# Kernel optimization log

Measured on AMD Instinct MI355X. Metric: run time of the kernel, lower is better.

Reference implementation:

```python
import jax, jax.numpy as jnp
import numpy as np
import math

EMBED = 256
NH = 8      # num_heads
NP = 4      # num_points
HD = EMBED // NH  # head_dim = 32
BS = 8
NQ = 8192
HH = 128
WW = 128


def setup_inputs() -> dict:
    key = jax.random.key(0)
    ks = jax.random.split(key, 12)
    query = jax.random.normal(ks[0], (BS, NQ, EMBED), jnp.float32)
    reference_points = jax.random.uniform(ks[1], (BS, NQ, 2), dtype=jnp.float32)
    value = jax.random.normal(ks[2], (BS, HH * WW, EMBED), jnp.float32)
    # sampling_offsets: torch init uses zero weight + structured bias (rose pattern);
    # use small random weight so the math path is exercised, keep the structured bias.
    w_off = 0.001 * jax.random.normal(ks[3], (EMBED, NH * NP * 2), jnp.float32)
    thetas = np.arange(NH, dtype=np.float32) * (2.0 * math.pi / NH)
    grid = np.stack([np.cos(thetas), np.sin(thetas)], -1)          # [NH, 2]
    grid = np.tile(grid[:, None, :], (1, NP, 1)) * np.arange(1, NP + 1, dtype=np.float32)[None, :, None]
    b_off = jnp.asarray(grid.reshape(-1), jnp.float32)              # [NH*NP*2]
    w_attn = 0.01 * jax.random.normal(ks[4], (EMBED, NH * NP), jnp.float32)
    b_attn = jnp.zeros((NH * NP,), jnp.float32)
    xav = 1.0 / math.sqrt(EMBED)
    w_val = xav * jax.random.normal(ks[5], (EMBED, EMBED), jnp.float32)
    b_val = jnp.zeros((EMBED,), jnp.float32)
    w_out = xav * jax.random.normal(ks[6], (EMBED, EMBED), jnp.float32)
    b_out = jnp.zeros((EMBED,), jnp.float32)
    return {"query": query, "reference_points": reference_points, "value": value,
            "w_off": w_off, "b_off": b_off, "w_attn": w_attn, "b_attn": b_attn,
            "w_val": w_val, "b_val": b_val, "w_out": w_out, "b_out": b_out,
            "H": HH, "W": WW}


def _deform_attn(query, reference_points, value, w_off, b_off, w_attn, b_attn,
                 w_val, b_val, w_out, b_out, H, W):
    bs, nq, _ = query.shape
    # value projection -> [bs, nh, H*W, hd]
    v = (value @ w_val + b_val).reshape(bs, H * W, NH, HD).transpose(0, 2, 1, 3)
    # offsets and attention weights
    off = (query @ w_off + b_off).reshape(bs, nq, NH, NP, 2)
    attn = jax.nn.softmax((query @ w_attn + b_attn).reshape(bs, nq, NH, NP), axis=-1)
    norm = jnp.array([W, H], dtype=query.dtype)
    loc = reference_points[:, :, None, None, :] + off / norm       # [bs,nq,nh,np,2] in [0,1]
    # grid_sample, align_corners=False: pixel = loc*size - 0.5  (x <-> W, y <-> H)
    px = (loc[..., 0] * W - 0.5).transpose(0, 2, 1, 3).reshape(bs, NH, nq * NP)
    py = (loc[..., 1] * H - 0.5).transpose(0, 2, 1, 3).reshape(bs, NH, nq * NP)
    x0 = jnp.floor(px); y0 = jnp.floor(py)
    wx = px - x0; wy = py - y0
    x0i = x0.astype(jnp.int32); y0i = y0.astype(jnp.int32)

    def gather(xi, yi):
        # padding_mode='zeros': out-of-range corners contribute 0
        mask = ((xi >= 0) & (xi < W) & (yi >= 0) & (yi < H)).astype(v.dtype)
        idx = jnp.clip(yi, 0, H - 1) * W + jnp.clip(xi, 0, W - 1)   # [bs,nh,K]
        g = jnp.take_along_axis(v, idx[..., None], axis=2)          # [bs,nh,K,hd]
        return g * mask[..., None]

    samp = (((1 - wx) * (1 - wy))[..., None] * gather(x0i, y0i)
            + (wx * (1 - wy))[..., None] * gather(x0i + 1, y0i)
            + ((1 - wx) * wy)[..., None] * gather(x0i, y0i + 1)
            + (wx * wy)[..., None] * gather(x0i + 1, y0i + 1))      # [bs,nh,nq*np,hd]
    samp = samp.reshape(bs, NH, nq, NP, HD)
    aw = attn.transpose(0, 2, 1, 3)                                 # [bs,nh,nq,np]
    out = jnp.einsum('bhqpd,bhqp->bqhd', samp, aw).reshape(bs, nq, EMBED)
    return out @ w_out + b_out


def reference(query, reference_points, value, w_off, b_off, w_attn, b_attn,
              w_val, b_val, w_out, b_out, H, W):
    return _deform_attn(query, reference_points, value, w_off, b_off, w_attn, b_attn,
                        w_val, b_val, w_out, b_out, H, W)
```

## Files before the change

kernel.cpp:

```cpp
#include <hip/hip_runtime.h>
#include <stdint.h>

#define NQ 8192
#define BSZ 8
#define NH 8
#define NP 4
#define HD 32
#define EMBED 256
#define IMG 128
#define NPIX (IMG*IMG)

typedef __attribute__((ext_vector_type(8))) short short8v;
typedef __attribute__((ext_vector_type(4))) float f32x4;

static __device__ __forceinline__ float bf2f(uint32_t u) {
    union { uint32_t i; float f; } x; x.i = u << 16; return x.f;
}
static __device__ __forceinline__ uint16_t f2bf(float f) {
    union { float f; uint32_t i; } x; x.f = f;
    uint32_t r = x.i + 0x7fffu + ((x.i >> 16) & 1u);
    return (uint16_t)(r >> 16);
}
static __device__ __forceinline__ uint32_t cvtpk(float lo, float hi) {
    uint32_t r;
    asm("v_cvt_pk_bf16_f32 %0, %1, %2" : "=v"(r) : "v"(lo), "v"(hi));
    return r;
}
static __device__ __forceinline__ void gload_lds16(const void* g, void* l) {
    __builtin_amdgcn_global_load_lds(
        (const __attribute__((address_space(1))) unsigned int*)g,
        (__attribute__((address_space(3))) unsigned int*)l, 16, 0, 0);
}

#define WAITV(n) asm volatile("s_waitcnt vmcnt(" #n ")" ::: "memory")
#define WAITLGKM() do { asm volatile("s_waitcnt lgkmcnt(0)" ::: "memory"); \
                        __builtin_amdgcn_sched_barrier(0); } while (0)
#define BARRIER() do { __builtin_amdgcn_s_barrier(); \
                       __builtin_amdgcn_sched_barrier(0); } while (0)

static __device__ __forceinline__ void waitv_n(int n) {
    switch (n) {
        case 0: WAITV(0); break;  case 1: WAITV(1); break;
        case 2: WAITV(2); break;  case 3: WAITV(3); break;
        case 4: WAITV(4); break;  case 5: WAITV(5); break;
        case 6: WAITV(6); break;  case 8: WAITV(8); break;
        default: WAITV(10); break;
    }
}

__global__ void pack_w(const float* __restrict__ w_val, const float* __restrict__ w_out,
                       const float* __restrict__ w_off, const float* __restrict__ w_attn,
                       uint16_t* __restrict__ wTval, uint16_t* __restrict__ wTout,
                       uint16_t* __restrict__ wTcat) {
    int k = blockIdx.x;
    int n = threadIdx.x;
    wTval[n * 256 + k] = f2bf(w_val[k * 256 + n]);
    wTout[n * 256 + k] = f2bf(w_out[k * 256 + n]);
    if (n < 64)       wTcat[n * 256 + k]        = f2bf(w_off[k * 64 + n]);
    else if (n < 96)  wTcat[n * 256 + k]        = f2bf(w_attn[k * 32 + (n - 64)]);
}

template<bool A_F32, bool OUT_F32, bool PLANE, int STRIPES>
__global__ __launch_bounds__(512, 2)
void gemm_pk(const void* __restrict__ Ap, const uint16_t* __restrict__ BT,
             void* __restrict__ Cp, const float* __restrict__ bias) {
    constexpr int TILEB = A_F32 ? 16384 : 8192;
    constexpr int NR    = 131072 / TILEB;
    constexpr int T     = STRIPES * 4;
    constexpr int LPT   = A_F32 ? 2 : 1;
    __shared__ char SMEM[131072 + (PLANE ? 32768 : 0)];
    char* ring = SMEM;
    const int tid = threadIdx.x, w = tid >> 6, l = tid & 63;
    const int stripe0 = blockIdx.x * STRIPES;

    auto stageA = [&](int slot, int t) {
        const int gr0 = (stripe0 + (t >> 2)) * 64 + (t & 3) * 16;
        if constexpr (A_F32) {
#pragma unroll
            for (int c = 0; c < 2; ++c) {
                int loff = c * 8192 + tid * 16;
                int row = loff >> 10, x = loff & 1023;
                const char* src = (const char*)Ap + (size_t)(gr0 + row) * 1024
                                  + (x ^ ((row & 7) << 4));
                gload_lds16(src, ring + slot * 16384 + c * 8192 + w * 1024);
            }
        } else {
            int loff = tid * 16;
            int row = loff >> 9, x = loff & 511;
            const char* src = (const char*)Ap + (size_t)(gr0 + row) * 512
                              + (x ^ ((row & 7) << 4));
            gload_lds16(src, ring + slot * 8192 + w * 1024);
        }
    };

#pragma unroll
    for (int c = 0; c < 16; ++c) {
        int loff = c * 8192 + tid * 16;
        int row = loff >> 9, x = loff & 511;
        const char* src = (const char*)BT + (size_t)row * 512 + (x ^ ((row & 7) << 4));
        gload_lds16(src, SMEM + c * 8192 + w * 1024);
    }
    WAITV(0);
    BARRIER();
    short8v breg[2][8];
#pragma unroll
    for (int n = 0; n < 2; ++n) {
        int col = w * 32 + n * 16 + (l & 15);
        const char* base = SMEM + col * 512;
        const int sz = (col & 7) << 4;
#pragma unroll
        for (int k = 0; k < 8; ++k)
            breg[n][k] = *(const short8v*)(base + ((k * 64 + (l >> 4) * 16) ^ sz));
    }
    WAITLGKM();
    BARRIER();
#pragma unroll
    for (int t = 0; t < 6; ++t) stageA(t & (NR - 1), t);

    for (int st = 0; st < STRIPES; ++st) {
        f32x4 acc[4][2] = {};
#pragma unroll
        for (int s = 0; s < 4; ++s) {
            const int t = st * 4 + s;
            const int rem = T - 1 - t;
            waitv_n((rem < 5 ? rem : 5) * LPT);
            BARRIER();
            if (t + 6 < T) stageA((t + 6) & (NR - 1), t + 6);
            const int slot = t & (NR - 1);
            short8v a[8];
            const int sz = (l & 7) << 4;
            if constexpr (A_F32) {
                const char* base = ring + slot * 16384 + (l & 15) * 1024;
#pragma unroll
                for (int k = 0; k < 8; ++k) {
                    int off = k * 128 + (l >> 4) * 32;
                    f32x4 lo = *(const f32x4*)(base + (off ^ sz));
                    f32x4 hi = *(const f32x4*)(base + ((off + 16) ^ sz));
                    union { uint32_t u[4]; short8v s8; } pk;
                    pk.u[0] = cvtpk(lo[0], lo[1]); pk.u[1] = cvtpk(lo[2], lo[3]);
                    pk.u[2] = cvtpk(hi[0], hi[1]); pk.u[3] = cvtpk(hi[2], hi[3]);
                    a[k] = pk.s8;
                }
            } else {
                const char* base = ring + slot * 8192 + (l & 15) * 512;
#pragma unroll
                for (int k = 0; k < 8; ++k)
                    a[k] = *(const short8v*)(base + ((k * 64 + (l >> 4) * 16) ^ sz));
            }
#pragma unroll
            for (int k = 0; k < 8; ++k)
#pragma unroll
                for (int n = 0; n < 2; ++n)
                    acc[s][n] = __builtin_amdgcn_mfma_f32_16x16x32_bf16(a[k], breg[n][k], acc[s][n], 0, 0, 0);
        }

        const int gr0 = (stripe0 + st) * 64;
        if constexpr (PLANE) {
            char* Cs = SMEM + 131072;
#pragma unroll
            for (int s = 0; s < 4; ++s)
#pragma unroll
                for (int n = 0; n < 2; ++n) {
                    int lcol = w * 32 + n * 16 + (l & 15);
                    float bv = bias[lcol];
#pragma unroll
                    for (int r = 0; r < 4; ++r) {
                        int lrow = s * 16 + (l >> 4) * 4 + r;
                        *(uint16_t*)(Cs + ((lrow * 512 + lcol * 2) ^ ((lrow & 7) << 4)))
                            = f2bf(acc[s][n][r] + bv);
                    }
                }
            WAITLGKM();
            BARRIER();
            const int b_ = gr0 >> 14, pix0 = gr0 & 16383;
            const int hg = tid >> 6, li = tid & 63;
            char* pb = (char*)Cp + (((size_t)(b_ * 8 + hg)) << 20) + (size_t)pix0 * 64;
#pragma unroll
            for (int i = 0; i < 4; ++i) {
                int fb = i * 1024 + li * 16;
                int lrow = fb >> 6, x = hg * 64 + (fb & 63);
                uint4 d = *(const uint4*)(Cs + ((lrow * 512 + x) ^ ((lrow & 7) << 4)));
                *(uint4*)(pb + (size_t)lrow * 64 + (fb & 63)) = d;
            }
        } else {
#pragma unroll
            for (int s = 0; s < 4; ++s)
#pragma unroll
                for (int n = 0; n < 2; ++n) {
                    int col = w * 32 + n * 16 + (l & 15);
                    float bv = bias[col];
#pragma unroll
                    for (int r = 0; r < 4; ++r) {
                        int gr = gr0 + s * 16 + (l >> 4) * 4 + r;
                        float val = acc[s][n][r] + bv;
                        if constexpr (OUT_F32)
                            ((float*)Cp)[(size_t)gr * 256 + col] = val;
                        else
                            ((uint16_t*)Cp)[(size_t)gr * 256 + col] = f2bf(val);
                    }
                }
        }
    }
}

__global__ __launch_bounds__(256, 2)
void proj_kernel(const float* __restrict__ Q, const uint16_t* __restrict__ WTcat,
                 const float* __restrict__ b_off, const float* __restrict__ b_attn,
                 const float* __restrict__ refp,
                 float* __restrict__ locs, float* __restrict__ attnw) {
    __shared__ uint16_t Bs[96 * 256];
    __shared__ uint16_t As[64 * 256];
    const int tid = threadIdx.x, w = tid >> 6, l = tid & 63;
    const int blk = blockIdx.x;

#pragma unroll
    for (int c = 0; c < 12; ++c) {
        int loff = (w * 12 + c) * 1024;
        int lofl = loff + l * 16;
        int row = lofl >> 9, colb = lofl & 511;
        const char* src = (const char*)WTcat + (size_t)row * 512 + (colb ^ ((row & 7) << 4));
        gload_lds16(src, (char*)Bs + loff);
    }
#pragma unroll
    for (int c = 0; c < 8; ++c) {
        int loff = tid * 16 + c * 4096;
        int row = loff >> 9, colb = loff & 511;
        const float* src = Q + (size_t)(blk * 64 + row) * 256 + (colb >> 1);
        float4 f0 = *(const float4*)src;
        float4 f1 = *(const float4*)(src + 4);
        uint4 pk;
        pk.x = (uint32_t)f2bf(f0.x) | ((uint32_t)f2bf(f0.y) << 16);
        pk.y = (uint32_t)f2bf(f0.z) | ((uint32_t)f2bf(f0.w) << 16);
        pk.z = (uint32_t)f2bf(f1.x) | ((uint32_t)f2bf(f1.y) << 16);
        pk.w = (uint32_t)f2bf(f1.z) | ((uint32_t)f2bf(f1.w) << 16);
        *(uint4*)((char*)As + row * 512 + (colb ^ ((row & 7) << 4))) = pk;
    }
    __syncthreads();

    f32x4 acc[6] = {};
    const int arow = w * 16 + (l & 15);
#pragma unroll
    for (int ks = 0; ks < 8; ++ks) {
        const int kb = ks * 64 + (l >> 4) * 16;
        short8v a = *(const short8v*)((const char*)As + arow * 512 + (kb ^ ((arow & 7) << 4)));
#pragma unroll
        for (int n = 0; n < 6; ++n) {
            int col = n * 16 + (l & 15);
            short8v b = *(const short8v*)((const char*)Bs + col * 512 + (kb ^ ((col & 7) << 4)));
            acc[n] = __builtin_amdgcn_mfma_f32_16x16x32_bf16(a, b, acc[n], 0, 0, 0);
        }
    }
    __syncthreads();
    float* scores = (float*)As;
#pragma unroll
    for (int n = 0; n < 6; ++n)
#pragma unroll
        for (int r = 0; r < 4; ++r)
            scores[(w * 16 + (l >> 4) * 4 + r) * 96 + n * 16 + (l & 15)] = acc[n][r];
    __syncthreads();

    for (int it = tid; it < 512; it += 256) {
        int row = it >> 3, h = it & 7;
        int gq = blk * 64 + row;
        int b = gq >> 13, q = gq & 8191;
        size_t itemH = ((size_t)(b * 8 + h) << 13) | q;
        float s0 = scores[row * 96 + 64 + h * 4 + 0] + b_attn[h * 4 + 0];
        float s1 = scores[row * 96 + 64 + h * 4 + 1] + b_attn[h * 4 + 1];
        float s2 = scores[row * 96 + 64 + h * 4 + 2] + b_attn[h * 4 + 2];
        float s3 = scores[row * 96 + 64 + h * 4 + 3] + b_attn[h * 4 + 3];
        float mx = fmaxf(fmaxf(s0, s1), fmaxf(s2, s3));
        float e0 = __expf(s0 - mx), e1 = __expf(s1 - mx);
        float e2 = __expf(s2 - mx), e3 = __expf(s3 - mx);
        float inv = 1.0f / (e0 + e1 + e2 + e3);
        float rx = refp[gq * 2 + 0] * 128.0f - 0.5f;
        float ry = refp[gq * 2 + 1] * 128.0f - 0.5f;
        float ew[4] = { e0, e1, e2, e3 };
#pragma unroll
        for (int p = 0; p < 4; ++p) {
            float ox = scores[row * 96 + h * 8 + p * 2 + 0] + b_off[h * 8 + p * 2 + 0];
            float oy = scores[row * 96 + h * 8 + p * 2 + 1] + b_off[h * 8 + p * 2 + 1];
            locs[itemH * 8 + p * 2 + 0] = rx + ox;
            locs[itemH * 8 + p * 2 + 1] = ry + oy;
            attnw[itemH * 4 + p] = ew[p] * inv;
        }
    }
}

__global__ __launch_bounds__(256)
void sample_kernel(const uint16_t* __restrict__ v, const float* __restrict__ locs,
                   const float* __restrict__ attnw, uint16_t* __restrict__ oatt) {
    const int bid = blockIdx.x;
    const int h = bid & 7;
    const int rest = bid >> 3;
    const int b = rest >> 7;
    const int chunk = rest & 127;
    const int qloc = threadIdx.x >> 2;
    const int dg = threadIdx.x & 3;
    const int q = chunk * 64 + qloc;
    const size_t itemH = ((size_t)(b * 8 + h) << 13) | q;
    const char* plane = (const char*)v + ((size_t)(b * 8 + h) << 20);

    float4 l01 = ((const float4*)locs)[itemH * 2 + 0];
    float4 l23 = ((const float4*)locs)[itemH * 2 + 1];
    float4 aw4 = ((const float4*)attnw)[itemH];
    float pxs[4] = { l01.x, l01.z, l23.x, l23.z };
    float pys[4] = { l01.y, l01.w, l23.y, l23.w };
    float aws[4] = { aw4.x, aw4.y, aw4.z, aw4.w };

    float acc[8] = {};
#pragma unroll
    for (int p = 0; p < 4; ++p) {
        float px = pxs[p], py = pys[p], aw = aws[p];
        float fx = floorf(px), fy = floorf(py);
        float wx = px - fx, wy = py - fy;
        int x0 = (int)fx, y0 = (int)fy;
#pragma unroll
        for (int cy = 0; cy < 2; ++cy) {
            int yy = y0 + cy;
            float wyv = cy ? wy : 1.f - wy;
            bool yok = (unsigned)yy < (unsigned)IMG;
            int yc = min(max(yy, 0), IMG - 1);
#pragma unroll
            for (int cx = 0; cx < 2; ++cx) {
                int xx = x0 + cx;
                bool ok = yok && ((unsigned)xx < (unsigned)IMG);
                int xc = min(max(xx, 0), IMG - 1);
                float wgt = ok ? aw * (cx ? wx : 1.f - wx) * wyv : 0.f;
                const uint4 u = *(const uint4*)(plane + ((size_t)(yc * IMG + xc) << 6) + dg * 16);
                acc[0] += wgt * bf2f(u.x & 0xffffu);
                acc[1] += wgt * bf2f(u.x >> 16);
                acc[2] += wgt * bf2f(u.y & 0xffffu);
                acc[3] += wgt * bf2f(u.y >> 16);
                acc[4] += wgt * bf2f(u.z & 0xffffu);
                acc[5] += wgt * bf2f(u.z >> 16);
                acc[6] += wgt * bf2f(u.w & 0xffffu);
                acc[7] += wgt * bf2f(u.w >> 16);
            }
        }
    }
    const size_t bq = (size_t)b * NQ + q;
    uint4 out;
    out.x = (uint32_t)f2bf(acc[0]) | ((uint32_t)f2bf(acc[1]) << 16);
    out.y = (uint32_t)f2bf(acc[2]) | ((uint32_t)f2bf(acc[3]) << 16);
    out.z = (uint32_t)f2bf(acc[4]) | ((uint32_t)f2bf(acc[5]) << 16);
    out.w = (uint32_t)f2bf(acc[6]) | ((uint32_t)f2bf(acc[7]) << 16);
    *(uint4*)((char*)oatt + (bq * 256 + h * 32 + dg * 8) * 2) = out;
}

extern "C" void kernel_launch(void* const* d_in, const int* in_sizes, int n_in,
                              void* d_out, int out_size, void* d_ws, size_t ws_size,
                              hipStream_t stream) {
    const float* query  = (const float*)d_in[0];
    const float* refp   = (const float*)d_in[1];
    const float* value  = (const float*)d_in[2];
    const float* w_off  = (const float*)d_in[3];
    const float* b_off  = (const float*)d_in[4];
    const float* w_attn = (const float*)d_in[5];
    const float* b_attn = (const float*)d_in[6];
    const float* w_val  = (const float*)d_in[7];
    const float* b_val  = (const float*)d_in[8];
    const float* w_out  = (const float*)d_in[9];
    const float* b_out  = (const float*)d_in[10];

    char* ws = (char*)d_ws;
    uint16_t* v     = (uint16_t*)(ws);
    uint16_t* oatt  = (uint16_t*)(ws + 67108864);
    float*    locs  = (float*)(ws + 100663296);
    float*    attnw = (float*)(ws + 117440512);
    uint16_t* wTval = (uint16_t*)(ws + 125829120);
    uint16_t* wTout = (uint16_t*)(ws + 125960192);
    uint16_t* wTcat = (uint16_t*)(ws + 126091264);

    pack_w<<<256, 256, 0, stream>>>(w_val, w_out, w_off, w_attn, wTval, wTout, wTcat);
    gemm_pk<true, false, true, 8><<<256, 512, 0, stream>>>(value, wTval, v, b_val);
    proj_kernel<<<1024, 256, 0, stream>>>(query, wTcat, b_off, b_attn, refp, locs, attnw);
    sample_kernel<<<8192, 256, 0, stream>>>(v, locs, attnw, oatt);
    gemm_pk<false, true, false, 4><<<256, 512, 0, stream>>>(oatt, wTout, (float*)d_out, b_out);
}
```

Before: 140.6 us.

## Convert fp32 A tiles to bf16 in registers before LDS staging

For fp32 inputs, the GEMM now loads A rows into registers with a two-deep software prefetch, packs them to bf16 and writes pre-packed tiles to LDS. Previously raw fp32 went to LDS via direct global-to-LDS loads and was converted on every fragment read. This halves LDS footprint per tile, drops the XOR swizzle and conversion from the MFMA inner loop, and gives a 16-slot ring. In exchange, global-load latency is hidden only by a short register prefetch, and a barrier is added after the plane write-out.

Result: no change. 142.9 us (+1.7%).

```diff
diff --git a/kernel.cpp b/kernel.cpp
--- a/kernel.cpp
+++ b/kernel.cpp
@@ -42,9 +42,7 @@
     switch (n) {
         case 0: WAITV(0); break;  case 1: WAITV(1); break;
         case 2: WAITV(2); break;  case 3: WAITV(3); break;
-        case 4: WAITV(4); break;  case 5: WAITV(5); break;
-        case 6: WAITV(6); break;  case 8: WAITV(8); break;
-        default: WAITV(10); break;
+        case 4: WAITV(4); break;  default: WAITV(5); break;
     }
 }
 
@@ -64,34 +62,34 @@
 __global__ __launch_bounds__(512, 2)
 void gemm_pk(const void* __restrict__ Ap, const uint16_t* __restrict__ BT,
              void* __restrict__ Cp, const float* __restrict__ bias) {
-    constexpr int TILEB = A_F32 ? 16384 : 8192;
-    constexpr int NR    = 131072 / TILEB;
-    constexpr int T     = STRIPES * 4;
-    constexpr int LPT   = A_F32 ? 2 : 1;
+    constexpr int T = STRIPES * 4;
     __shared__ char SMEM[131072 + (PLANE ? 32768 : 0)];
     char* ring = SMEM;
     const int tid = threadIdx.x, w = tid >> 6, l = tid & 63;
     const int stripe0 = blockIdx.x * STRIPES;
 
-    auto stageA = [&](int slot, int t) {
-        const int gr0 = (stripe0 + (t >> 2)) * 64 + (t & 3) * 16;
-        if constexpr (A_F32) {
-#pragma unroll
-            for (int c = 0; c < 2; ++c) {
-                int loff = c * 8192 + tid * 16;
-                int row = loff >> 10, x = loff & 1023;
-                const char* src = (const char*)Ap + (size_t)(gr0 + row) * 1024
-                                  + (x ^ ((row & 7) << 4));
-                gload_lds16(src, ring + slot * 16384 + c * 8192 + w * 1024);
-            }
-        } else {
-            int loff = tid * 16;
-            int row = loff >> 9, x = loff & 511;
-            const char* src = (const char*)Ap + (size_t)(gr0 + row) * 512
-                              + (x ^ ((row & 7) << 4));
-            gload_lds16(src, ring + slot * 8192 + w * 1024);
-        }
+    auto grow0 = [&](int t) { return (stripe0 + (t >> 2)) * 64 + (t & 3) * 16; };
+
+    auto loadA = [&](int t, float4 (&fb)[2]) {
+        const char* src = (const char*)Ap + (size_t)(grow0(t) + (tid & 15)) * 1024
+                          + (tid >> 4) * 32;
+        fb[0] = ((const float4*)src)[0];
+        fb[1] = ((const float4*)src)[1];
     };
+    auto writeA = [&](int t, const float4 (&fb)[2]) {
+        uint4 pk;
+        pk.x = cvtpk(fb[0].x, fb[0].y); pk.y = cvtpk(fb[0].z, fb[0].w);
+        pk.z = cvtpk(fb[1].x, fb[1].y); pk.w = cvtpk(fb[1].z, fb[1].w);
+        *(uint4*)(ring + (t & 15) * 8192 + tid * 16) = pk;
+    };
+    auto stageA_lds = [&](int t) {
+        const char* src = (const char*)Ap + (size_t)(grow0(t) + (l & 15)) * 512
+                          + (l >> 4) * 16 + w * 64;
+        gload_lds16(src, ring + (t & 15) * 8192 + w * 1024);
+    };
+
+    float4 fbuf[2][2];
+    if constexpr (A_F32) { loadA(0, fbuf[0]); loadA(1, fbuf[1]); }
 
 #pragma unroll
     for (int c = 0; c < 16; ++c) {
@@ -114,39 +112,34 @@
     }
     WAITLGKM();
     BARRIER();
-#pragma unroll
-    for (int t = 0; t < 6; ++t) stageA(t & (NR - 1), t);
+    if constexpr (A_F32) {
+        writeA(0, fbuf[0]);
+    } else {
+#pragma unroll
+        for (int t = 0; t < 6; ++t) stageA_lds(t);
+    }
 
     for (int st = 0; st < STRIPES; ++st) {
         f32x4 acc[4][2] = {};
 #pragma unroll
         for (int s = 0; s < 4; ++s) {
             const int t = st * 4 + s;
-            const int rem = T - 1 - t;
-            waitv_n((rem < 5 ? rem : 5) * LPT);
-            BARRIER();
-            if (t + 6 < T) stageA((t + 6) & (NR - 1), t + 6);
-            const int slot = t & (NR - 1);
+            if constexpr (A_F32) {
+                if (t + 2 < T) loadA(t + 2, fbuf[s & 1]);
+                if (t + 1 < T) writeA(t + 1, fbuf[(s + 1) & 1]);
+                WAITLGKM();
+                BARRIER();
+            } else {
+                const int rem = T - 1 - t;
+                waitv_n(rem < 5 ? rem : 5);
+                BARRIER();
+                if (t + 6 < T) stageA_lds(t + 6);
+            }
+            const char* abase = ring + (t & 15) * 8192 + l * 16;
             short8v a[8];
-            const int sz = (l & 7) << 4;
-            if constexpr (A_F32) {
-                const char* base = ring + slot * 16384 + (l & 15) * 1024;
-#pragma unroll
-                for (int k = 0; k < 8; ++k) {
-                    int off = k * 128 + (l >> 4) * 32;
-                    f32x4 lo = *(const f32x4*)(base + (off ^ sz));
-                    f32x4 hi = *(const f32x4*)(base + ((off + 16) ^ sz));
-                    union { uint32_t u[4]; short8v s8; } pk;
-                    pk.u[0] = cvtpk(lo[0], lo[1]); pk.u[1] = cvtpk(lo[2], lo[3]);
-                    pk.u[2] = cvtpk(hi[0], hi[1]); pk.u[3] = cvtpk(hi[2], hi[3]);
-                    a[k] = pk.s8;
-                }
-            } else {
-                const char* base = ring + slot * 8192 + (l & 15) * 512;
-#pragma unroll
-                for (int k = 0; k < 8; ++k)
-                    a[k] = *(const short8v*)(base + ((k * 64 + (l >> 4) * 16) ^ sz));
-            }
+#pragma unroll
+            for (int k = 0; k < 8; ++k)
+                a[k] = *(const short8v*)(abase + k * 1024);
 #pragma unroll
             for (int k = 0; k < 8; ++k)
 #pragma unroll
@@ -173,15 +166,16 @@
             WAITLGKM();
             BARRIER();
             const int b_ = gr0 >> 14, pix0 = gr0 & 16383;
-            const int hg = tid >> 6, li = tid & 63;
-            char* pb = (char*)Cp + (((size_t)(b_ * 8 + hg)) << 20) + (size_t)pix0 * 64;
+            char* pb = (char*)Cp + (((size_t)(b_ * 8 + w)) << 20) + (size_t)pix0 * 64;
 #pragma unroll
             for (int i = 0; i < 4; ++i) {
-                int fb = i * 1024 + li * 16;
-                int lrow = fb >> 6, x = hg * 64 + (fb & 63);
+                int fb = i * 1024 + l * 16;
+                int lrow = fb >> 6, x = w * 64 + (fb & 63);
                 uint4 d = *(const uint4*)(Cs + ((lrow * 512 + x) ^ ((lrow & 7) << 4)));
                 *(uint4*)(pb + (size_t)lrow * 64 + (fb & 63)) = d;
             }
+            WAITLGKM();
+            BARRIER();
         } else {
 #pragma unroll
             for (int s = 0; s < 4; ++s)
```
